# Kernel tuning notes

Measured on AMD Instinct MI355X. Metric: run time of the kernel, lower is better.

Reference implementation:

```python
import jax, jax.numpy as jnp
import numpy as np

B, U = 64, 512            # batch, max_units
AE = 1024
UE = 256                  # unit_embedding_size
A = 256                   # target_head_attention_size


def setup_inputs() -> dict:
    key = jax.random.key(0)
    ks = jax.random.split(key, 10)
    return {
        "autoregressive_embedding": jax.random.normal(ks[0], (B, U, AE), jnp.float32),
        "own_unit_embeddings": jax.random.normal(ks[1], (B, U, UE), jnp.float32),
        "enemy_unit_embeddings": jax.random.normal(ks[2], (B, U, UE), jnp.float32),
        "nr_own_units": jax.random.randint(ks[3], (B, 1), 0, U).astype(jnp.int64),
        "nr_units_enemy": jax.random.randint(ks[4], (B, 1), 0, U).astype(jnp.int64),
        "nr_own_flags": jax.random.randint(ks[5], (B, 1), 0, 8).astype(jnp.int64),
        "Wq": jax.random.normal(ks[6], (UE + AE, A), jnp.float32) * (1.0 / np.sqrt(UE + AE)),
        "bq": jnp.zeros((A,), jnp.float32),
        "Wk": jax.random.normal(ks[7], (UE, A), jnp.float32) * (1.0 / np.sqrt(UE)),
        "bk": jnp.zeros((A,), jnp.float32),
    }


def reference(autoregressive_embedding, own_unit_embeddings, enemy_unit_embeddings,
              nr_own_units, nr_units_enemy, nr_own_flags, Wq, bq, Wk, bk):
    # combined: [B, U, AE+UE]
    combined = jnp.concatenate([autoregressive_embedding, own_unit_embeddings], axis=2)
    queries = combined @ Wq + bq                       # [B, U, A]
    keys = enemy_unit_embeddings @ Wk + bk             # [B, U, A]
    attention = jnp.einsum("bqd,bkd->bqk", queries, keys) / (A ** 0.5)  # [B, U, U]
    # Vectorized mask: rows in [nr_own_flags, nr_own_units), cols in [0, nr_units_enemy)
    idx = jnp.arange(U)
    row_ok = (idx[None, :] >= nr_own_flags) & (idx[None, :] < nr_own_units)  # [B, U]
    col_ok = idx[None, :] < nr_units_enemy                                   # [B, U]
    mask = jnp.where(row_ok[:, :, None] & col_ok[:, None, :], 1.0, 1e-9)     # [B, U, U]
    return jax.nn.softmax(attention * mask, axis=-1)
```

## Files before the change

kernel.cpp:

```cpp
#include <hip/hip_runtime.h>

constexpr int B  = 64;
constexpr int U  = 512;
constexpr int AE = 1024;
constexpr int UE = 256;
constexpr int A  = 256;
constexpr int KQ = AE + UE;

typedef _Float16 f16x8 __attribute__((ext_vector_type(8)));
typedef float    f32x4 __attribute__((ext_vector_type(4)));

__global__ void prep(const float* __restrict__ Wq, const float* __restrict__ Wk,
                     _Float16* __restrict__ WqT, _Float16* __restrict__ WkT) {
    int idx = blockIdx.x * 256 + threadIdx.x;
    if (idx < KQ * A) {
        int k = idx >> 8, n = idx & 255;
        WqT[(size_t)n * KQ + k] = (_Float16)Wq[idx];
    } else {
        int j = idx - KQ * A;
        if (j < A * A) {
            int k = j >> 8, n = j & 255;
            WkT[(size_t)n * A + k] = (_Float16)Wk[j];
        }
    }
}

__global__ __launch_bounds__(512, 1) void gemm(
    const float* __restrict__ A1, int s1, int split,
    const float* __restrict__ A2, int s2,
    const _Float16* __restrict__ BT,
    const float* __restrict__ bias,
    _Float16* __restrict__ Out,
    int Ktot)
{
    __shared__ __align__(16) _Float16 Al[2][128][32];
    __shared__ __align__(16) _Float16 Bl[2][256][32];

    const int t    = threadIdx.x;
    const int lane = t & 63;
    const int w    = t >> 6;
    const int lm   = lane & 15;
    const int mbase = blockIdx.x * 128;

    const int wm = (w & 1) * 64;
    const int wn = (w >> 1) * 64;

    f32x4 acc[4][4] = {};

    const int ar = t >> 2;
    const int as = t & 3;
    const int ap = as >> 1;
    const size_t garow = mbase + ar;

    const int br = t >> 1;
    const int bs = t & 1;

    float4 aR[4];
    f16x8  bR[4];

    auto loadA = [&](int k0) {
        int kg = k0 + as * 16;
        const float* src = (kg < split) ? (A1 + garow * (size_t)s1 + kg)
                                        : (A2 + garow * (size_t)s2 + (kg - split));
        aR[0] = ((const float4*)src)[0];
        aR[1] = ((const float4*)src)[1];
        aR[2] = ((const float4*)src)[2];
        aR[3] = ((const float4*)src)[3];
    };
    auto loadB = [&](int k0) {
        const _Float16* src = BT + (size_t)br * Ktot + k0 + bs * 32;
        bR[0] = ((const f16x8*)src)[0];
        bR[1] = ((const f16x8*)src)[1];
        bR[2] = ((const f16x8*)src)[2];
        bR[3] = ((const f16x8*)src)[3];
    };

    loadA(0);
    loadB(0);

    const int rsw = (lm >> 1) & 3;
    const int nk = Ktot >> 6;
    for (int kb = 0; kb < nk; kb++) {
        __syncthreads();
        {
            #pragma unroll
            for (int j = 0; j < 2; j++) {
                const float4 x = aR[j * 2], y = aR[j * 2 + 1];
                f16x8 hv;
                hv[0] = (_Float16)x.x; hv[1] = (_Float16)x.y;
                hv[2] = (_Float16)x.z; hv[3] = (_Float16)x.w;
                hv[4] = (_Float16)y.x; hv[5] = (_Float16)y.y;
                hv[6] = (_Float16)y.z; hv[7] = (_Float16)y.w;
                int c = (as & 1) * 2 + j;
                *(f16x8*)(&Al[ap][ar][(c ^ ((ar >> 1) & 3)) * 8]) = hv;
            }
            #pragma unroll
            for (int j = 0; j < 4; j++)
                *(f16x8*)(&Bl[bs][br][(j ^ ((br >> 1) & 3)) * 8]) = bR[j];
        }
        __syncthreads();
        if (kb + 1 < nk) { loadA(kb * 64 + 64); loadB(kb * 64 + 64); }
        #pragma unroll
        for (int p = 0; p < 2; p++) {
            f16x8 af[4], bf[4];
            #pragma unroll
            for (int mt = 0; mt < 4; mt++)
                af[mt] = *(const f16x8*)(&Al[p][wm + mt * 16 + lm][((lane >> 4) ^ rsw) * 8]);
            #pragma unroll
            for (int nt = 0; nt < 4; nt++)
                bf[nt] = *(const f16x8*)(&Bl[p][wn + nt * 16 + lm][((lane >> 4) ^ rsw) * 8]);
            #pragma unroll
            for (int mt = 0; mt < 4; mt++)
                #pragma unroll
                for (int nt = 0; nt < 4; nt++)
                    acc[mt][nt] = __builtin_amdgcn_mfma_f32_16x16x32_f16(
                        af[mt], bf[nt], acc[mt][nt], 0, 0, 0);
        }
    }

    const int rsub = (lane >> 4) * 4;
    #pragma unroll
    for (int nt = 0; nt < 4; nt++) {
        const int col = wn + nt * 16 + lm;
        const float bv = bias[col];
        const int c5 = col >> 5, c31 = col & 31;
        #pragma unroll
        for (int mt = 0; mt < 4; mt++)
            #pragma unroll
            for (int r = 0; r < 4; r++) {
                int row = mbase + wm + mt * 16 + rsub + r;
                int bb = row >> 9, u = row & 511;
                Out[(((size_t)bb * 8 + c5) * 512 + u) * 32 + c31] =
                    (_Float16)(acc[mt][nt][r] + bv);
            }
    }
}

__global__ __launch_bounds__(512, 2) void attn(
    const _Float16* __restrict__ Qh, const _Float16* __restrict__ Kh,
    const int* __restrict__ nr_own_units, const int* __restrict__ nr_units_enemy,
    const int* __restrict__ nr_own_flags, float* __restrict__ Out)
{
    __shared__ __align__(16) _Float16 Ql[8][64][32];
    __shared__ __align__(16) _Float16 Kl[512][32];
    __shared__ float red[64][4];

    const int t    = threadIdx.x;
    const int lane = t & 63;
    const int w    = t >> 6;
    const int lm   = lane & 15;
    const int b    = blockIdx.y;
    const int qbase = blockIdx.x * 64;

    const int wm = (w & 1) * 32;
    const int wn = (w >> 1) * 128;

    const int nf = nr_own_flags[b];
    const int nu = nr_own_units[b];
    const int ne = nr_units_enemy[b];

    {
        f16x8 qreg[4];
        #pragma unroll
        for (int j = 0; j < 4; j++) {
            int s = j * 512 + t;
            int p = s >> 8, row = (s & 255) >> 2, cq = s & 3;
            qreg[j] = *(const f16x8*)(Qh + (((size_t)b * 8 + p) * 512 + qbase + row) * 32 + cq * 8);
        }
        #pragma unroll
        for (int j = 0; j < 4; j++) {
            int s = j * 512 + t;
            int p = s >> 8, row = (s & 255) >> 2, cq = s & 3;
            *(f16x8*)(&Ql[p][row][(cq ^ ((row >> 1) & 3)) * 8]) = qreg[j];
        }
    }

    const _Float16* Kb = Kh + (size_t)b * 8 * 512 * 32;
    f16x8 kreg[4];
    auto loadK = [&](int c) {
        const _Float16* src = Kb + ((size_t)c * 512 + t) * 32;
        kreg[0] = ((const f16x8*)src)[0];
        kreg[1] = ((const f16x8*)src)[1];
        kreg[2] = ((const f16x8*)src)[2];
        kreg[3] = ((const f16x8*)src)[3];
    };
    loadK(0);

    f32x4 acc[2][8] = {};
    const int rsw = (lm >> 1) & 3;
    for (int c = 0; c < 8; c++) {
        __syncthreads();
        #pragma unroll
        for (int j = 0; j < 4; j++)
            *(f16x8*)(&Kl[t][(j ^ ((t >> 1) & 3)) * 8]) = kreg[j];
        __syncthreads();
        if (c < 7) loadK(c + 1);
        f16x8 af[2], bf[8];
        #pragma unroll
        for (int mt = 0; mt < 2; mt++)
            af[mt] = *(const f16x8*)(&Ql[c][wm + mt * 16 + lm][((lane >> 4) ^ rsw) * 8]);
        #pragma unroll
        for (int nt = 0; nt < 8; nt++)
            bf[nt] = *(const f16x8*)(&Kl[wn + nt * 16 + lm][((lane >> 4) ^ rsw) * 8]);
        #pragma unroll
        for (int mt = 0; mt < 2; mt++)
            #pragma unroll
            for (int nt = 0; nt < 8; nt++)
                acc[mt][nt] = __builtin_amdgcn_mfma_f32_16x16x32_f16(
                    af[mt], bf[nt], acc[mt][nt], 0, 0, 0);
    }

    const int rsub = (lane >> 4) * 4;
    #pragma unroll
    for (int mt = 0; mt < 2; mt++)
        #pragma unroll
        for (int nt = 0; nt < 8; nt++)
            #pragma unroll
            for (int r = 0; r < 4; r++) {
                int uq = qbase + wm + mt * 16 + rsub + r;
                int col = wn + nt * 16 + lm;
                bool ok = (col < ne) && (uq >= nf) && (uq < nu);
                acc[mt][nt][r] = acc[mt][nt][r] * 0.0625f * (ok ? 1.0f : 1e-9f);
            }

    float mx[2][4];
    #pragma unroll
    for (int mt = 0; mt < 2; mt++)
        #pragma unroll
        for (int r = 0; r < 4; r++) {
            float m = acc[mt][0][r];
            #pragma unroll
            for (int nt = 1; nt < 8; nt++) m = fmaxf(m, acc[mt][nt][r]);
            #pragma unroll
            for (int off = 1; off <= 8; off <<= 1) m = fmaxf(m, __shfl_xor(m, off));
            mx[mt][r] = m;
        }
    if (lm == 0) {
        #pragma unroll
        for (int mt = 0; mt < 2; mt++)
            #pragma unroll
            for (int r = 0; r < 4; r++)
                red[wm + mt * 16 + rsub + r][w >> 1] = mx[mt][r];
    }
    __syncthreads();
    #pragma unroll
    for (int mt = 0; mt < 2; mt++)
        #pragma unroll
        for (int r = 0; r < 4; r++) {
            f32x4 v = *(const f32x4*)(&red[wm + mt * 16 + rsub + r][0]);
            mx[mt][r] = fmaxf(fmaxf(v[0], v[1]), fmaxf(v[2], v[3]));
        }
    __syncthreads();

    float sm[2][4];
    #pragma unroll
    for (int mt = 0; mt < 2; mt++)
        #pragma unroll
        for (int r = 0; r < 4; r++) {
            float s = 0.f;
            #pragma unroll
            for (int nt = 0; nt < 8; nt++) {
                float e = __expf(acc[mt][nt][r] - mx[mt][r]);
                acc[mt][nt][r] = e;
                s += e;
            }
            #pragma unroll
            for (int off = 1; off <= 8; off <<= 1) s += __shfl_xor(s, off);
            sm[mt][r] = s;
        }
    if (lm == 0) {
        #pragma unroll
        for (int mt = 0; mt < 2; mt++)
            #pragma unroll
            for (int r = 0; r < 4; r++)
                red[wm + mt * 16 + rsub + r][w >> 1] = sm[mt][r];
    }
    __syncthreads();

    #pragma unroll
    for (int mt = 0; mt < 2; mt++)
        #pragma unroll
        for (int r = 0; r < 4; r++) {
            int rl = wm + mt * 16 + rsub + r;
            f32x4 v = *(const f32x4*)(&red[rl][0]);
            float inv = 1.0f / (v[0] + v[1] + v[2] + v[3]);
            float* orow = Out + ((size_t)b * 512 + qbase + rl) * 512 + wn + lm;
            #pragma unroll
            for (int nt = 0; nt < 8; nt++)
                orow[nt * 16] = acc[mt][nt][r] * inv;
        }
}

extern "C" void kernel_launch(void* const* d_in, const int* in_sizes, int n_in,
                              void* d_out, int out_size, void* d_ws, size_t ws_size,
                              hipStream_t stream) {
    const float* ar    = (const float*)d_in[0];
    const float* own   = (const float*)d_in[1];
    const float* enemy = (const float*)d_in[2];
    const int*   n_own   = (const int*)d_in[3];
    const int*   n_enemy = (const int*)d_in[4];
    const int*   n_flags = (const int*)d_in[5];
    const float* Wq = (const float*)d_in[6];
    const float* bq = (const float*)d_in[7];
    const float* Wk = (const float*)d_in[8];
    const float* bk = (const float*)d_in[9];
    float* out = (float*)d_out;

    char* ws = (char*)d_ws;
    _Float16* WqT = (_Float16*)(ws);
    _Float16* WkT = (_Float16*)(ws + 655360);
    _Float16* Qh  = (_Float16*)(ws + 786432);
    _Float16* Kh  = (_Float16*)(ws + 786432 + 16777216);

    prep<<<dim3((KQ * A + A * A) / 256), dim3(256), 0, stream>>>(Wq, Wk, WqT, WkT);

    gemm<<<dim3(256), dim3(512), 0, stream>>>(ar, AE, AE, own, UE, WqT, bq, Qh, KQ);
    gemm<<<dim3(256), dim3(512), 0, stream>>>(enemy, UE, 0, enemy, UE, WkT, bk, Kh, A);

    attn<<<dim3(8, B), dim3(512), 0, stream>>>(Qh, Kh, n_own, n_enemy, n_flags, out);
}
```

Before: 333.1 us.

## Double-buffer LDS tiles, stage GEMM and softmax outputs through LDS for vector stores

The GEMM and attention kernels now ping-pong two LDS buffers, so each K-step needs one barrier instead of two. The GEMM epilogue writes results to an LDS tile and then stores 16-byte vectors to the blocked Q/K layout, replacing scattered 2-byte stores. The attention epilogue stages normalized probabilities per wave in LDS and writes float4 rows to the output, where it previously did strided scalar stores. The GEMM is also templated on K and split, and launch bounds change to allow 2 blocks per CU, at the cost of more LDS and extra epilogue barriers.

```diff
diff --git a/kernel.cpp b/kernel.cpp
--- a/kernel.cpp
+++ b/kernel.cpp
@@ -8,6 +8,7 @@
 constexpr int KQ = AE + UE;
 
 typedef _Float16 f16x8 __attribute__((ext_vector_type(8)));
+typedef _Float16 f16x4 __attribute__((ext_vector_type(4)));
 typedef float    f32x4 __attribute__((ext_vector_type(4)));
 
 __global__ void prep(const float* __restrict__ Wq, const float* __restrict__ Wk,
@@ -25,90 +26,84 @@
     }
 }
 
-__global__ __launch_bounds__(512, 1) void gemm(
-    const float* __restrict__ A1, int s1, int split,
+template<int KTOT, int SPLIT>
+__global__ __launch_bounds__(512, 2) void gemm(
+    const float* __restrict__ A1, int s1,
     const float* __restrict__ A2, int s2,
     const _Float16* __restrict__ BT,
     const float* __restrict__ bias,
-    _Float16* __restrict__ Out,
-    int Ktot)
+    _Float16* __restrict__ Out)
 {
-    __shared__ __align__(16) _Float16 Al[2][128][32];
-    __shared__ __align__(16) _Float16 Bl[2][256][32];
+    __shared__ __align__(16) char smem[98304];
+    _Float16 (*Ab)[128][64] = (_Float16(*)[128][64])smem;
+    _Float16 (*Bb)[256][64] = (_Float16(*)[256][64])(smem + 32768);
+    _Float16 (*Cl)[264]     = (_Float16(*)[264])smem;
 
     const int t    = threadIdx.x;
     const int lane = t & 63;
     const int w    = t >> 6;
     const int lm   = lane & 15;
     const int mbase = blockIdx.x * 128;
-
     const int wm = (w & 1) * 64;
     const int wn = (w >> 1) * 64;
 
     f32x4 acc[4][4] = {};
 
-    const int ar = t >> 2;
-    const int as = t & 3;
-    const int ap = as >> 1;
-    const size_t garow = mbase + ar;
-
-    const int br = t >> 1;
-    const int bs = t & 1;
+    const int arow = t >> 2, aseg = t & 3;
+    const size_t ga = mbase + arow;
+    const int brow = t >> 1, bseg = t & 1;
 
     float4 aR[4];
     f16x8  bR[4];
-
     auto loadA = [&](int k0) {
-        int kg = k0 + as * 16;
-        const float* src = (kg < split) ? (A1 + garow * (size_t)s1 + kg)
-                                        : (A2 + garow * (size_t)s2 + (kg - split));
-        aR[0] = ((const float4*)src)[0];
-        aR[1] = ((const float4*)src)[1];
-        aR[2] = ((const float4*)src)[2];
-        aR[3] = ((const float4*)src)[3];
+        int kg = k0 + aseg * 16;
+        const float* s = (kg < SPLIT) ? (A1 + ga * (size_t)s1 + kg)
+                                      : (A2 + ga * (size_t)s2 + (kg - SPLIT));
+        aR[0] = ((const float4*)s)[0]; aR[1] = ((const float4*)s)[1];
+        aR[2] = ((const float4*)s)[2]; aR[3] = ((const float4*)s)[3];
     };
     auto loadB = [&](int k0) {
-        const _Float16* src = BT + (size_t)br * Ktot + k0 + bs * 32;
-        bR[0] = ((const f16x8*)src)[0];
-        bR[1] = ((const f16x8*)src)[1];
-        bR[2] = ((const f16x8*)src)[2];
-        bR[3] = ((const f16x8*)src)[3];
+        const _Float16* s = BT + (size_t)brow * KTOT + k0 + bseg * 32;
+        bR[0] = ((const f16x8*)s)[0]; bR[1] = ((const f16x8*)s)[1];
+        bR[2] = ((const f16x8*)s)[2]; bR[3] = ((const f16x8*)s)[3];
     };
 
-    loadA(0);
-    loadB(0);
-
-    const int rsw = (lm >> 1) & 3;
-    const int nk = Ktot >> 6;
+    loadA(0); loadB(0);
+
+    constexpr int nk = KTOT / 64;
     for (int kb = 0; kb < nk; kb++) {
+        const int bi = kb & 1;
+        #pragma unroll
+        for (int j = 0; j < 2; j++) {
+            const float4 x = aR[2 * j], y = aR[2 * j + 1];
+            f16x8 hv;
+            hv[0] = (_Float16)x.x; hv[1] = (_Float16)x.y;
+            hv[2] = (_Float16)x.z; hv[3] = (_Float16)x.w;
+            hv[4] = (_Float16)y.x; hv[5] = (_Float16)y.y;
+            hv[6] = (_Float16)y.z; hv[7] = (_Float16)y.w;
+            int c = aseg * 2 + j;
+            *(f16x8*)(&Ab[bi][arow][(c ^ (arow & 7)) * 8]) = hv;
+        }
+        #pragma unroll
+        for (int j = 0; j < 4; j++) {
+            int c = bseg * 4 + j;
+            *(f16x8*)(&Bb[bi][brow][(c ^ (brow & 7)) * 8]) = bR[j];
+        }
         __syncthreads();
-        {
-            #pragma unroll
-            for (int j = 0; j < 2; j++) {
-                const float4 x = aR[j * 2], y = aR[j * 2 + 1];
-                f16x8 hv;
-                hv[0] = (_Float16)x.x; hv[1] = (_Float16)x.y;
-                hv[2] = (_Float16)x.z; hv[3] = (_Float16)x.w;
-                hv[4] = (_Float16)y.x; hv[5] = (_Float16)y.y;
-                hv[6] = (_Float16)y.z; hv[7] = (_Float16)y.w;
-                int c = (as & 1) * 2 + j;
-                *(f16x8*)(&Al[ap][ar][(c ^ ((ar >> 1) & 3)) * 8]) = hv;
-            }
-            #pragma unroll
-            for (int j = 0; j < 4; j++)
-                *(f16x8*)(&Bl[bs][br][(j ^ ((br >> 1) & 3)) * 8]) = bR[j];
-        }
-        __syncthreads();
-        if (kb + 1 < nk) { loadA(kb * 64 + 64); loadB(kb * 64 + 64); }
+        if (kb + 1 < nk) { loadA((kb + 1) * 64); loadB((kb + 1) * 64); }
         #pragma unroll
         for (int p = 0; p < 2; p++) {
             f16x8 af[4], bf[4];
             #pragma unroll
-            for (int mt = 0; mt < 4; mt++)
-                af[mt] = *(const f16x8*)(&Al[p][wm + mt * 16 + lm][((lane >> 4) ^ rsw) * 8]);
-            #pragma unroll
-            for (int nt = 0; nt < 4; nt++)
-                bf[nt] = *(const f16x8*)(&Bl[p][wn + nt * 16 + lm][((lane >> 4) ^ rsw) * 8]);
+            for (int mt = 0; mt < 4; mt++) {
+                int r = wm + mt * 16 + lm;
+                af[mt] = *(const f16x8*)(&Ab[bi][r][((p * 4 + (lane >> 4)) ^ (r & 7)) * 8]);
+            }
+            #pragma unroll
+            for (int nt = 0; nt < 4; nt++) {
+                int r = wn + nt * 16 + lm;
+                bf[nt] = *(const f16x8*)(&Bb[bi][r][((p * 4 + (lane >> 4)) ^ (r & 7)) * 8]);
+            }
             #pragma unroll
             for (int mt = 0; mt < 4; mt++)
                 #pragma unroll
@@ -118,21 +113,29 @@
         }
     }
 
+    __syncthreads();
     const int rsub = (lane >> 4) * 4;
     #pragma unroll
     for (int nt = 0; nt < 4; nt++) {
         const int col = wn + nt * 16 + lm;
         const float bv = bias[col];
-        const int c5 = col >> 5, c31 = col & 31;
         #pragma unroll
         for (int mt = 0; mt < 4; mt++)
             #pragma unroll
-            for (int r = 0; r < 4; r++) {
-                int row = mbase + wm + mt * 16 + rsub + r;
-                int bb = row >> 9, u = row & 511;
-                Out[(((size_t)bb * 8 + c5) * 512 + u) * 32 + c31] =
-                    (_Float16)(acc[mt][nt][r] + bv);
-            }
+            for (int r = 0; r < 4; r++)
+                Cl[wm + mt * 16 + rsub + r][col] = (_Float16)(acc[mt][nt][r] + bv);
+    }
+    __syncthreads();
+    const int bb = mbase >> 9, u0 = mbase & 511;
+    const int uu = t >> 2, q = t & 3;
+    #pragma unroll
+    for (int c5 = 0; c5 < 8; c5++) {
+        f16x4 v0 = *(const f16x4*)(&Cl[uu][c5 * 32 + q * 8]);
+        f16x4 v1 = *(const f16x4*)(&Cl[uu][c5 * 32 + q * 8 + 4]);
+        f16x8 v;
+        v[0]=v0[0]; v[1]=v0[1]; v[2]=v0[2]; v[3]=v0[3];
+        v[4]=v1[0]; v[5]=v1[1]; v[6]=v1[2]; v[7]=v1[3];
+        *(f16x8*)(Out + (((size_t)bb * 8 + c5) * 512 + u0 + uu) * 32 + q * 8) = v;
     }
 }
 
@@ -141,8 +144,9 @@
     const int* __restrict__ nr_own_units, const int* __restrict__ nr_units_enemy,
     const int* __restrict__ nr_own_flags, float* __restrict__ Out)
 {
-    __shared__ __align__(16) _Float16 Ql[8][64][32];
-    __shared__ __align__(16) _Float16 Kl[512][32];
+    __shared__ __align__(16) char smem[98304];
+    _Float16 (*Ql)[64][32]  = (_Float16(*)[64][32])smem;
+    _Float16 (*Kl)[512][32] = (_Float16(*)[512][32])(smem + 32768);
     __shared__ float red[64][4];
 
     const int t    = threadIdx.x;
@@ -171,37 +175,38 @@
         for (int j = 0; j < 4; j++) {
             int s = j * 512 + t;
             int p = s >> 8, row = (s & 255) >> 2, cq = s & 3;
-            *(f16x8*)(&Ql[p][row][(cq ^ ((row >> 1) & 3)) * 8]) = qreg[j];
+            *(f16x8*)(&Ql[p][row][(cq ^ (row & 3)) * 8]) = qreg[j];
         }
     }
 
     const _Float16* Kb = Kh + (size_t)b * 8 * 512 * 32;
     f16x8 kreg[4];
     auto loadK = [&](int c) {
-        const _Float16* src = Kb + ((size_t)c * 512 + t) * 32;
-        kreg[0] = ((const f16x8*)src)[0];
-        kreg[1] = ((const f16x8*)src)[1];
-        kreg[2] = ((const f16x8*)src)[2];
-        kreg[3] = ((const f16x8*)src)[3];
+        const _Float16* s = Kb + ((size_t)c * 512 + t) * 32;
+        kreg[0] = ((const f16x8*)s)[0]; kreg[1] = ((const f16x8*)s)[1];
+        kreg[2] = ((const f16x8*)s)[2]; kreg[3] = ((const f16x8*)s)[3];
     };
     loadK(0);
 
     f32x4 acc[2][8] = {};
-    const int rsw = (lm >> 1) & 3;
     for (int c = 0; c < 8; c++) {
-        __syncthreads();
+        const int bi = c & 1;
         #pragma unroll
         for (int j = 0; j < 4; j++)
-            *(f16x8*)(&Kl[t][(j ^ ((t >> 1) & 3)) * 8]) = kreg[j];
+            *(f16x8*)(&Kl[bi][t][(j ^ (t & 3)) * 8]) = kreg[j];
         __syncthreads();
         if (c < 7) loadK(c + 1);
         f16x8 af[2], bf[8];
         #pragma unroll
-        for (int mt = 0; mt < 2; mt++)
-            af[mt] = *(const f16x8*)(&Ql[c][wm + mt * 16 + lm][((lane >> 4) ^ rsw) * 8]);
-        #pragma unroll
-        for (int nt = 0; nt < 8; nt++)
-            bf[nt] = *(const f16x8*)(&Kl[wn + nt * 16 + lm][((lane >> 4) ^ rsw) * 8]);
+        for (int mt = 0; mt < 2; mt++) {
+            int r = wm + mt * 16 + lm;
+            af[mt] = *(const f16x8*)(&Ql[c][r][((lane >> 4) ^ (r & 3)) * 8]);
+        }
+        #pragma unroll
+        for (int nt = 0; nt < 8; nt++) {
+            int r = wn + nt * 16 + lm;
+            bf[nt] = *(const f16x8*)(&Kl[bi][r][((lane >> 4) ^ (r & 3)) * 8]);
+        }
         #pragma unroll
         for (int mt = 0; mt < 2; mt++)
             #pragma unroll
@@ -235,13 +240,12 @@
             for (int off = 1; off <= 8; off <<= 1) m = fmaxf(m, __shfl_xor(m, off));
             mx[mt][r] = m;
         }
-    if (lm == 0) {
+    if (lm == 0)
         #pragma unroll
         for (int mt = 0; mt < 2; mt++)
             #pragma unroll
             for (int r = 0; r < 4; r++)
                 red[wm + mt * 16 + rsub + r][w >> 1] = mx[mt][r];
-    }
     __syncthreads();
     #pragma unroll
     for (int mt = 0; mt < 2; mt++)
@@ -268,27 +272,44 @@
             for (int off = 1; off <= 8; off <<= 1) s += __shfl_xor(s, off);
             sm[mt][r] = s;
         }
-    if (lm == 0) {
+    if (lm == 0)
         #pragma unroll
         for (int mt = 0; mt < 2; mt++)
             #pragma unroll
             for (int r = 0; r < 4; r++)
                 red[wm + mt * 16 + rsub + r][w >> 1] = sm[mt][r];
-    }
-    __syncthreads();
-
+    __syncthreads();
+
+    float inv[2][4];
     #pragma unroll
     for (int mt = 0; mt < 2; mt++)
         #pragma unroll
         for (int r = 0; r < 4; r++) {
-            int rl = wm + mt * 16 + rsub + r;
-            f32x4 v = *(const f32x4*)(&red[rl][0]);
-            float inv = 1.0f / (v[0] + v[1] + v[2] + v[3]);
-            float* orow = Out + ((size_t)b * 512 + qbase + rl) * 512 + wn + lm;
-            #pragma unroll
-            for (int nt = 0; nt < 8; nt++)
-                orow[nt * 16] = acc[mt][nt][r] * inv;
-        }
+            f32x4 v = *(const f32x4*)(&red[wm + mt * 16 + rsub + r][0]);
+            inv[mt][r] = 1.0f / (v[0] + v[1] + v[2] + v[3]);
+        }
+    __syncthreads();
+
+    float* Sw = (float*)(smem + w * 8448);
+    #pragma unroll
+    for (int mt = 0; mt < 2; mt++) {
+        #pragma unroll
+        for (int nt = 0; nt < 8; nt++)
+            #pragma unroll
+            for (int r = 0; r < 4; r++)
+                Sw[(rsub + r) * 132 + nt * 16 + lm] = acc[mt][nt][r] * inv[mt][r];
+        const int srow = lane >> 5;
+        const int scol = (lane & 31) * 4;
+        #pragma unroll
+        for (int pass = 0; pass < 8; pass++) {
+            int row = pass * 2 + srow;
+            float2 a0 = *(const float2*)(&Sw[row * 132 + scol]);
+            float2 a1 = *(const float2*)(&Sw[row * 132 + scol + 2]);
+            float4 v; v.x = a0.x; v.y = a0.y; v.z = a1.x; v.w = a1.y;
+            *(float4*)(Out + ((size_t)b * 512 + qbase + wm + mt * 16 + row) * 512
+                           + wn + scol) = v;
+        }
+    }
 }
 
 extern "C" void kernel_launch(void* const* d_in, const int* in_sizes, int n_in,
@@ -314,8 +335,8 @@
 
     prep<<<dim3((KQ * A + A * A) / 256), dim3(256), 0, stream>>>(Wq, Wk, WqT, WkT);
 
-    gemm<<<dim3(256), dim3(512), 0, stream>>>(ar, AE, AE, own, UE, WqT, bq, Qh, KQ);
-    gemm<<<dim3(256), dim3(512), 0, stream>>>(enemy, UE, 0, enemy, UE, WkT, bk, Kh, A);
+    gemm<KQ, AE><<<dim3(256), dim3(512), 0, stream>>>(ar, AE, own, UE, WqT, bq, Qh);
+    gemm<A, 0><<<dim3(256), dim3(512), 0, stream>>>(enemy, UE, enemy, UE, WkT, bk, Kh);
 
     attn<<<dim3(8, B), dim3(512), 0, stream>>>(Qh, Kh, n_own, n_enemy, n_flags, out);
 }
```

Result: slower. 340.5 us (+2.2%).
